# Optimization experiments

Measured on AMD Instinct MI355X. Metric: run time of the kernel, lower is better.

## Reference

```python
import jax, jax.numpy as jnp
import numpy as np

D_MODEL = 2048
HEADS = 32
HEAD_DIM = 64   # D_MODEL // HEADS
STATE = 256
KCONV = 4
CHUNK = 64
EPS = 1e-5
CONV_DIM = D_MODEL + 2 * STATE          # 2560 (n_groups=1)
PROJ = D_MODEL + CONV_DIM + HEADS       # 4640 (z | xBC | dt)
BATCH, SEQ = 2, 2048


def rmsnorm(x, w, eps=EPS):
    return x * jax.lax.rsqrt(jnp.mean(x * x, axis=-1, keepdims=True) + eps) * w


def setup_inputs() -> dict:
    key = jax.random.key(0)
    ks = jax.random.split(key, 8)
    x = jax.random.normal(ks[0], (BATCH, SEQ, D_MODEL), jnp.float32)
    norm_w = jnp.ones((D_MODEL,), jnp.float32)
    w_in = jax.random.normal(ks[1], (D_MODEL, PROJ), jnp.float32) * 0.02
    conv_w = jax.random.normal(ks[2], (CONV_DIM, KCONV), jnp.float32) * 0.2
    conv_b = jnp.zeros((CONV_DIM,), jnp.float32)
    # HF-style dt init: softplus(dt_bias) uniform-log in [1e-3, 1e-1]
    dt0 = jnp.exp(jax.random.uniform(ks[3], (HEADS,)) * (np.log(0.1) - np.log(0.001)) + np.log(0.001))
    dt_bias = dt0 + jnp.log(-jnp.expm1(-dt0))
    A_log = jnp.log(jnp.arange(1, HEADS + 1, dtype=jnp.float32))
    D_skip = jnp.ones((HEADS,), jnp.float32)
    gnorm_w = jnp.ones((D_MODEL,), jnp.float32)
    w_out = jax.random.normal(ks[4], (D_MODEL, D_MODEL), jnp.float32) * 0.02
    wo_w = jax.random.normal(ks[5], (D_MODEL, D_MODEL), jnp.float32) * 0.02
    return {"x": x, "norm_w": norm_w, "w_in": w_in, "conv_w": conv_w, "conv_b": conv_b,
            "dt_bias": dt_bias, "A_log": A_log, "D_skip": D_skip, "gnorm_w": gnorm_w,
            "w_out": w_out, "wo_w": wo_w}


def reference(x, norm_w, w_in, conv_w, conv_b, dt_bias, A_log, D_skip, gnorm_w, w_out, wo_w):
    b, L, _ = x.shape
    nc = L // CHUNK
    # pre-RMSNorm
    xn = rmsnorm(x, norm_w)
    # in_proj and split: z | xBC | dt
    proj = xn @ w_in
    z = proj[..., :D_MODEL]
    xBC = proj[..., D_MODEL:D_MODEL + CONV_DIM]
    dt = proj[..., D_MODEL + CONV_DIM:]                      # [b,L,H]
    # causal depthwise conv1d (kernel 4) + SiLU
    xp = jnp.pad(xBC, ((0, 0), (KCONV - 1, 0), (0, 0)))
    conv = conv_b + sum(xp[:, k:k + L] * conv_w[:, k] for k in range(KCONV))
    conv = jax.nn.silu(conv)
    xs = conv[..., :D_MODEL].reshape(b, L, HEADS, HEAD_DIM)  # SSM input
    Bm = conv[..., D_MODEL:D_MODEL + STATE]                  # [b,L,N] (n_groups=1)
    Cm = conv[..., D_MODEL + STATE:]                         # [b,L,N]
    dt = jax.nn.softplus(dt + dt_bias)                       # [b,L,H], >0
    A = -jnp.exp(A_log)                                      # [H]
    # ---- Mamba2 chunked selective scan (chunk_size=64) ----
    def ck(a):
        return a.reshape(b, nc, CHUNK, *a.shape[2:])
    xs_c, dt_c, B_c, C_c = ck(xs), ck(dt), ck(Bm), ck(Cm)
    Adt = dt_c * A                                           # [b,c,l,h] (<=0)
    Acs = jnp.cumsum(Adt, axis=2)
    # intra-chunk (diagonal blocks)
    seg = Acs[:, :, :, None, :] - Acs[:, :, None, :, :]      # [b,c,l,s,h]
    idx = jnp.arange(CHUNK)
    mask = (idx[:, None] >= idx[None, :])[None, None, :, :, None]
    Lmat = jnp.where(mask, jnp.exp(seg), 0.0)                # [b,c,l,s,h]
    CB = jnp.einsum('bcln,bcsn->bcls', C_c, B_c)
    xt = xs_c * dt_c[..., None]                              # [b,c,l,h,p]
    Y_diag = jnp.einsum('bclsh,bcshp->bclhp', CB[..., None] * Lmat, xt)
    # chunk-final states
    decay_states = jnp.exp(Acs[:, :, -1:, :] - Acs)          # [b,c,l,h]
    states = jnp.einsum('bcln,bclh,bclhp->bchpn', B_c, decay_states, xt)
    # inter-chunk recurrence (scan over nc chunks only)
    chunk_decay = jnp.exp(Acs[:, :, -1, :])                  # [b,c,h]
    def step(S, inp):
        dec, st = inp
        return S * dec[:, :, None, None] + st, S
    S0 = jnp.zeros((b, HEADS, HEAD_DIM, STATE), x.dtype)
    _, prev = jax.lax.scan(step, S0, (jnp.moveaxis(chunk_decay, 1, 0), jnp.moveaxis(states, 1, 0)))
    prev = jnp.moveaxis(prev, 0, 1)                          # [b,c,h,p,n] state at chunk start
    Y_off = jnp.einsum('bcln,bchpn,bclh->bclhp', C_c, prev, jnp.exp(Acs))
    y = (Y_diag + Y_off).reshape(b, L, HEADS, HEAD_DIM) + D_skip[None, None, :, None] * xs
    y = y.reshape(b, L, D_MODEL)
    # gated RMSNorm, out_proj, then wo
    y = rmsnorm(y * jax.nn.silu(z), gnorm_w)
    return (y @ w_out) @ wo_w
```

## Files before the change

kernel.cpp:

```cpp
#include <hip/hip_runtime.h>
#include <math.h>

#define D_MODEL 2048
#define HEADS 32
#define HEAD_DIM 64
#define STATE 256
#define KCONV 4
#define CHUNK 64
#define NC 32
#define SEQL 2048
#define BATCHN 2
#define CONV_DIMN 2560
#define PROJ_DIM 4640
#define PROJB_W 4608
#define EPSF 1e-5f
#define BL (BATCHN * SEQL)

typedef __attribute__((ext_vector_type(8))) short short8;
typedef __attribute__((ext_vector_type(4))) short short4v;
typedef __attribute__((ext_vector_type(4))) float f32x4;

__device__ __forceinline__ short f2bf(float f) {
  unsigned u = __builtin_bit_cast(unsigned, f);
  u = (u + 0x7fffu + ((u >> 16) & 1u)) >> 16;
  return (short)u;
}
__device__ __forceinline__ float b2f(short s) {
  unsigned u = ((unsigned)(unsigned short)s) << 16;
  return __builtin_bit_cast(float, u);
}
__device__ __forceinline__ void gld16(const void* g, void* l) {
  __builtin_amdgcn_global_load_lds((const __attribute__((address_space(1))) unsigned int*)g,
                                   (__attribute__((address_space(3))) unsigned int*)l,
                                   16, 0, 0);
}

__global__ __launch_bounds__(256) void transpose_bf16_k(const float* __restrict__ W,
                                                        short* __restrict__ WT,
                                                        int K, int ncols, int stride) {
  __shared__ float tile[32][33];
  int bn = blockIdx.x * 32, bk = blockIdx.y * 32;
  int tx = threadIdx.x & 31, ty = threadIdx.x >> 5;
  #pragma unroll
  for (int i = 0; i < 32; i += 8) {
    int k = bk + ty + i, n = bn + tx;
    tile[ty + i][tx] = (n < ncols) ? W[(size_t)k * stride + n] : 0.f;
  }
  __syncthreads();
  #pragma unroll
  for (int i = 0; i < 32; i += 8) {
    int n = bn + ty + i, k = bk + tx;
    WT[(size_t)n * K + k] = f2bf(tile[tx][ty + i]);
  }
}

__global__ __launch_bounds__(256) void dt_gemm_k(const float* __restrict__ x,
                                                 const float* __restrict__ norm_w,
                                                 const float* __restrict__ w_in,
                                                 short* __restrict__ xnb,
                                                 float* __restrict__ dtraw) {
  int row = blockIdx.x;
  int t = threadIdx.x;
  __shared__ float sx[D_MODEL];
  __shared__ float red[8][32];
  __shared__ float sred[4];
  const float4* x4 = (const float4*)(x + (size_t)row * D_MODEL);
  const float4* nw4 = (const float4*)norm_w;
  float ss = 0.f;
  for (int i = t; i < D_MODEL / 4; i += 256) {
    float4 v = x4[i];
    ss += v.x * v.x + v.y * v.y + v.z * v.z + v.w * v.w;
    float4 nw = nw4[i];
    float4 pv; pv.x = v.x * nw.x; pv.y = v.y * nw.y; pv.z = v.z * nw.z; pv.w = v.w * nw.w;
    ((float4*)sx)[i] = pv;
  }
  #pragma unroll
  for (int off = 32; off > 0; off >>= 1) ss += __shfl_down(ss, off);
  if ((t & 63) == 0) sred[t >> 6] = ss;
  __syncthreads();
  float tot = sred[0] + sred[1] + sred[2] + sred[3];
  float scale = rsqrtf(tot / (float)D_MODEL + EPSF);
  {
    float4 a = ((const float4*)sx)[2 * t], b = ((const float4*)sx)[2 * t + 1];
    short tmp[8];
    tmp[0] = f2bf(a.x * scale); tmp[1] = f2bf(a.y * scale);
    tmp[2] = f2bf(a.z * scale); tmp[3] = f2bf(a.w * scale);
    tmp[4] = f2bf(b.x * scale); tmp[5] = f2bf(b.y * scale);
    tmp[6] = f2bf(b.z * scale); tmp[7] = f2bf(b.w * scale);
    *(int4*)(xnb + (size_t)row * D_MODEL + t * 8) = *(int4*)tmp;
  }
  int h = t & 31, sl = t >> 5;
  float acc = 0.f;
  for (int k = sl * 256; k < sl * 256 + 256; k++)
    acc += sx[k] * w_in[(size_t)k * PROJ_DIM + (D_MODEL + CONV_DIMN) + h];
  red[sl][h] = acc;
  __syncthreads();
  if (t < 32) {
    float s = 0.f;
    #pragma unroll
    for (int i = 0; i < 8; i++) s += red[i][t];
    dtraw[(size_t)row * HEADS + t] = s * scale;
  }
}

template<bool BF16OUT>
__global__ __launch_bounds__(256, 2) void gemm_tw_k(const short* __restrict__ A,
                                                    const short* __restrict__ BT,
                                                    void* __restrict__ Cout,
                                                    int M, int N, int K) {
  constexpr int ABUF = 256 * 32;
  constexpr int BUFS = ABUF + 128 * 32;
  constexpr int LPT = 6;
  __shared__ short lds[3 * BUFS];

  const int t = threadIdx.x;
  const int lane = t & 63, w = t >> 6;
  const int mr = lane & 15, q = lane >> 4;
  const int cq8 = (q ^ ((mr >> 1) & 3)) * 8;
  const int stj = ((lane & 3) ^ ((lane >> 3) & 3)) * 8;
  const int str = lane >> 2;
  const int wm = w & 1, wn = w >> 1;

  const int nbx = N >> 7;
  const int nwg = nbx * (M >> 8);
  const int cpx = nwg >> 3;
  const int bid = blockIdx.x;
  const int swz = (bid & 7) * cpx + (bid >> 3);
  const int bx = swz % nbx, by = swz / nbx;
  const int m0 = by * 256, n0 = bx * 128;

  const int NT = K >> 5;
  f32x4 acc[8][4] = {};

  auto STAGE = [&](int tile, int buf) {
    short* dst = &lds[buf * BUFS];
    const int kb = tile * 32 + stj;
    #pragma unroll
    for (int cc = 0; cc < 4; cc++)
      gld16(A + (size_t)(m0 + w * 64 + cc * 16 + str) * K + kb,
            dst + (w * 64 + cc * 16) * 32);
    #pragma unroll
    for (int cc = 0; cc < 2; cc++)
      gld16(BT + (size_t)(n0 + w * 32 + cc * 16 + str) * K + kb,
            dst + ABUF + (w * 32 + cc * 16) * 32);
  };

  STAGE(0, 0); STAGE(1, 1);
  asm volatile("s_waitcnt vmcnt(%0)" :: "n"(LPT) : "memory");
  __builtin_amdgcn_s_barrier();

  int bufc = 0;
  for (int tt = 0; tt < NT; ++tt) {
    const short* sA = &lds[bufc * BUFS];
    const short* sB = sA + ABUF;
    if (tt + 2 < NT) STAGE(tt + 2, bufc >= 1 ? bufc - 1 : 2);
    short8 af[4], bfr[4];
    #pragma unroll
    for (int ni = 0; ni < 4; ni++)
      bfr[ni] = *(const short8*)&sB[(wn * 64 + ni * 16 + mr) * 32 + cq8];
    #pragma unroll
    for (int mi = 0; mi < 4; mi++)
      af[mi] = *(const short8*)&sA[(wm * 128 + mi * 16 + mr) * 32 + cq8];
    __builtin_amdgcn_s_setprio(1);
    #pragma unroll
    for (int mi = 0; mi < 4; mi++)
      #pragma unroll
      for (int ni = 0; ni < 4; ni++)
        acc[mi][ni] = __builtin_amdgcn_mfma_f32_16x16x32_bf16(af[mi], bfr[ni], acc[mi][ni], 0, 0, 0);
    __builtin_amdgcn_s_setprio(0);
    #pragma unroll
    for (int mi = 0; mi < 4; mi++)
      af[mi] = *(const short8*)&sA[(wm * 128 + 64 + mi * 16 + mr) * 32 + cq8];
    __builtin_amdgcn_s_setprio(1);
    #pragma unroll
    for (int mi = 0; mi < 4; mi++)
      #pragma unroll
      for (int ni = 0; ni < 4; ni++)
        acc[4 + mi][ni] = __builtin_amdgcn_mfma_f32_16x16x32_bf16(af[mi], bfr[ni], acc[4 + mi][ni], 0, 0, 0);
    __builtin_amdgcn_s_setprio(0);
    __builtin_amdgcn_sched_barrier(0);
    if (tt + 2 < NT) asm volatile("s_waitcnt vmcnt(%0)" :: "n"(LPT) : "memory");
    else             asm volatile("s_waitcnt vmcnt(0)" ::: "memory");
    __builtin_amdgcn_s_barrier();
    bufc = (bufc == 2) ? 0 : bufc + 1;
  }

  #pragma unroll
  for (int mi = 0; mi < 8; mi++)
    #pragma unroll
    for (int ni = 0; ni < 4; ni++) {
      const int gm = m0 + wm * 128 + ((mi & 3) + (mi >> 2) * 4) * 16 + ((mi >> 2) ? 64 - 64 : 0);
      const int gmr = m0 + wm * 128 + (mi >> 2) * 64 + (mi & 3) * 16 + q * 4;
      const int gn = n0 + wn * 64 + ni * 16 + mr;
      #pragma unroll
      for (int r = 0; r < 4; r++) {
        if (BF16OUT) ((short*)Cout)[(size_t)(gmr + r) * N + gn] = f2bf(acc[mi][ni][r]);
        else         ((float*)Cout)[(size_t)(gmr + r) * N + gn] = acc[mi][ni][r];
      }
    }
}

__global__ __launch_bounds__(256) void conv_silu_k(const short* __restrict__ projb,
                                                   const float* __restrict__ cw,
                                                   const float* __restrict__ cb,
                                                   short* __restrict__ out) {
  int idx = blockIdx.x * 256 + threadIdx.x;
  int ci = idx % (CONV_DIMN / 8);
  int bt = idx / (CONV_DIMN / 8);
  int t = bt & (SEQL - 1);
  int b = bt >> 11;
  int c = ci * 8;
  float4 w4[8];
  #pragma unroll
  for (int j = 0; j < 8; j++) w4[j] = ((const float4*)cw)[c + j];
  float acc[8];
  {
    float4 b0 = ((const float4*)(cb + c))[0], b1 = ((const float4*)(cb + c))[1];
    acc[0] = b0.x; acc[1] = b0.y; acc[2] = b0.z; acc[3] = b0.w;
    acc[4] = b1.x; acc[5] = b1.y; acc[6] = b1.z; acc[7] = b1.w;
  }
  #pragma unroll
  for (int k = 0; k < KCONV; k++) {
    int tt = t - (KCONV - 1) + k;
    if (tt < 0) continue;
    short8 v = *(const short8*)&projb[((size_t)(b * SEQL + tt)) * PROJB_W + D_MODEL + c];
    #pragma unroll
    for (int j = 0; j < 8; j++) {
      float wv = (k == 0) ? w4[j].x : (k == 1) ? w4[j].y : (k == 2) ? w4[j].z : w4[j].w;
      acc[j] += b2f(v[j]) * wv;
    }
  }
  short o[8];
  #pragma unroll
  for (int j = 0; j < 8; j++) o[j] = f2bf(acc[j] / (1.f + expf(-acc[j])));
  *(int4*)&out[(size_t)bt * CONV_DIMN + c] = *(int4*)o;
}

__global__ __launch_bounds__(256) void dt_acs_k(const float* __restrict__ dtraw,
                                                const float* __restrict__ dt_bias,
                                                const float* __restrict__ A_log,
                                                float* __restrict__ dtb, float* __restrict__ acsb) {
  int bc = blockIdx.x;
  int b = bc / NC, c = bc % NC;
  int t = threadIdx.x;
  int l = t & 63, w = t >> 6;
  size_t base = ((size_t)(b * SEQL + c * CHUNK + l)) * HEADS;
  #pragma unroll
  for (int i = 0; i < 8; i++) {
    int h = w * 8 + i;
    float raw = dtraw[base + h] + dt_bias[h];
    float dt = raw > 20.f ? raw : log1pf(expf(raw));
    float adt = -expf(A_log[h]) * dt;
    float cs = adt;
    #pragma unroll
    for (int off = 1; off < 64; off <<= 1) {
      float v = __shfl_up(cs, off);
      if (l >= off) cs += v;
    }
    dtb[base + h] = dt;
    acsb[base + h] = cs;
  }
}

__global__ __launch_bounds__(256) void cb_k(const short* __restrict__ convb,
                                            short* __restrict__ CB) {
  int bc = blockIdx.x;
  int b = bc / NC, c = bc % NC;
  __shared__ float sC[64][65];
  __shared__ float sB[64][65];
  int t = threadIdx.x;
  int s = t & 63;
  int lb = (t >> 6) * 16;
  float acc[16] = {};
  size_t rowb = ((size_t)(b * SEQL + c * CHUNK)) * CONV_DIMN;
  for (int nt = 0; nt < 4; nt++) {
    __syncthreads();
    #pragma unroll
    for (int i = 0; i < 16; i++) {
      int e = t + 256 * i;
      int r = e >> 6, col = e & 63;
      sC[r][col] = b2f(convb[rowb + (size_t)r * CONV_DIMN + (D_MODEL + STATE) + nt * 64 + col]);
      sB[r][col] = b2f(convb[rowb + (size_t)r * CONV_DIMN + D_MODEL + nt * 64 + col]);
    }
    __syncthreads();
    for (int n = 0; n < 64; n++) {
      float bv = sB[s][n];
      #pragma unroll
      for (int j = 0; j < 16; j++) acc[j] += sC[lb + j][n] * bv;
    }
  }
  size_t ob = ((size_t)bc) * 64 * 64;
  #pragma unroll
  for (int j = 0; j < 16; j++) CB[ob + (size_t)(lb + j) * 64 + s] = f2bf(acc[j]);
}

__global__ __launch_bounds__(256) void chunk_states_k(const short* __restrict__ convb,
                                                      const float* __restrict__ dtb,
                                                      const float* __restrict__ acsb,
                                                      short* __restrict__ G0,
                                                      short* __restrict__ G1) {
  int blk = blockIdx.x & 1023;
  int b = blockIdx.x >> 10;
  short* G = b ? G1 : G0;
  int h = blk & 31, c = blk >> 5;
  __shared__ __align__(16) short sXT[64][72];
  __shared__ __align__(16) short sBT[256][72];
  __shared__ float swt[64];
  int t = threadIdx.x;
  size_t rowb = ((size_t)(b * SEQL + c * CHUNK)) * CONV_DIMN;
  size_t ab = ((size_t)(b * SEQL + c * CHUNK)) * HEADS;
  if (t < 64) {
    float a = acsb[ab + (size_t)t * HEADS + h];
    float alast = acsb[ab + (size_t)63 * HEADS + h];
    swt[t] = expf(alast - a) * dtb[ab + (size_t)t * HEADS + h];
  }
  __syncthreads();
  #pragma unroll
  for (int i = 0; i < 4; i++) {
    int e = t + 256 * i;
    int l = e >> 4, p4 = (e & 15) * 4;
    short4v v = *(const short4v*)&convb[rowb + (size_t)l * CONV_DIMN + h * HEAD_DIM + p4];
    float wt = swt[l];
    short vv[4] = {v.x, v.y, v.z, v.w};
    #pragma unroll
    for (int j = 0; j < 4; j++) {
      int p = p4 + j;
      sXT[p][((((l >> 3) ^ ((p >> 2) & 7)) << 3) | (l & 7))] = f2bf(b2f(vv[j]) * wt);
    }
  }
  #pragma unroll
  for (int i = 0; i < 16; i++) {
    int e = t + 256 * i;
    int l = e >> 6, n4 = (e & 63) * 4;
    short4v v = *(const short4v*)&convb[rowb + (size_t)l * CONV_DIMN + D_MODEL + n4];
    short vv[4] = {v.x, v.y, v.z, v.w};
    #pragma unroll
    for (int j = 0; j < 4; j++) {
      int n = n4 + j;
      sBT[n][((((l >> 3) ^ ((n >> 2) & 7)) << 3) | (l & 7))] = vv[j];
    }
  }
  __syncthreads();
  int lane = t & 63, w = t >> 6;
  int mr = lane & 15, q = lane >> 4;
  f32x4 acc[4][4] = {};
  #pragma unroll
  for (int ks = 0; ks < 2; ks++) {
    short8 af[4], bfr[4];
    #pragma unroll
    for (int mi = 0; mi < 4; mi++) {
      int p = mi * 16 + mr;
      af[mi] = *(const short8*)&sXT[p][(((ks * 4 + q) ^ ((p >> 2) & 7)) << 3)];
    }
    #pragma unroll
    for (int ni = 0; ni < 4; ni++) {
      int n = w * 64 + ni * 16 + mr;
      bfr[ni] = *(const short8*)&sBT[n][(((ks * 4 + q) ^ ((n >> 2) & 7)) << 3)];
    }
    #pragma unroll
    for (int mi = 0; mi < 4; mi++)
      #pragma unroll
      for (int ni = 0; ni < 4; ni++)
        acc[mi][ni] = __builtin_amdgcn_mfma_f32_16x16x32_bf16(af[mi], bfr[ni], acc[mi][ni], 0, 0, 0);
  }
  size_t gb = (size_t)blk * (64 * 256);
  #pragma unroll
  for (int mi = 0; mi < 4; mi++)
    #pragma unroll
    for (int ni = 0; ni < 4; ni++)
      #pragma unroll
      for (int r = 0; r < 4; r++)
        G[gb + (size_t)(mi * 16 + q * 4 + r) * 256 + w * 64 + ni * 16 + mr] = f2bf(acc[mi][ni][r]);
}

__global__ __launch_bounds__(256) void scan_states_k(short* __restrict__ G0,
                                                     short* __restrict__ G1,
                                                     const float* __restrict__ acsb) {
  int gid = blockIdx.x * 256 + threadIdx.x;
  int b = gid >> 16;
  int tid = gid & 65535;
  short* G = b ? G1 : G0;
  int n8 = tid & 31, p = (tid >> 5) & 63, h = tid >> 11;
  float S[8] = {};
  for (int c = 0; c < NC; c++) {
    size_t base = (((size_t)(c * HEADS + h) * 64) + p) * 256 + n8 * 8;
    short gs[8];
    *(int4*)gs = *(const int4*)&G[base];
    short ws8[8];
    #pragma unroll
    for (int j = 0; j < 8; j++) ws8[j] = f2bf(S[j]);
    *(int4*)&G[base] = *(int4*)ws8;
    float dec = expf(acsb[((size_t)(b * SEQL + c * CHUNK + 63)) * HEADS + h]);
    #pragma unroll
    for (int j = 0; j < 8; j++) S[j] = S[j] * dec + b2f(gs[j]);
  }
}

__global__ __launch_bounds__(256) void y_fused_k(const short* __restrict__ convb,
                                                 const short* __restrict__ CBb,
                                                 const short* __restrict__ G0,
                                                 const short* __restrict__ G1,
                                                 const float* __restrict__ dtb,
                                                 const float* __restrict__ acsb,
                                                 const float* __restrict__ D_skip,
                                                 float* __restrict__ Y) {
  int blk = blockIdx.x & 1023;
  int b = blockIdx.x >> 10;
  const short* G = b ? G1 : G0;
  int h = blk & 31, c = blk >> 5;
  __shared__ __align__(16) short sM[64][72];
  __shared__ __align__(16) short sXT[64][72];
  __shared__ float sacs[64], sdt[64], sea[64];
  int t = threadIdx.x;
  int lane = t & 63, w = t >> 6;
  size_t rowb = ((size_t)(b * SEQL + c * CHUNK)) * CONV_DIMN;
  size_t ab = ((size_t)(b * SEQL + c * CHUNK)) * HEADS;
  size_t cbbase = ((size_t)(b * NC + c)) * 64 * 64;
  if (t < 64) {
    float a = acsb[ab + (size_t)t * HEADS + h];
    sacs[t] = a;
    sea[t] = expf(a);
    sdt[t] = dtb[ab + (size_t)t * HEADS + h];
  }
  __syncthreads();
  #pragma unroll
  for (int i = 0; i < 16; i++) {
    int e = t + 256 * i;
    int r = e >> 6, col = e & 63;
    float m = 0.f;
    if (col <= r)
      m = b2f(CBb[cbbase + (size_t)r * 64 + col]) * expf(sacs[r] - sacs[col]) * sdt[col];
    sM[r][col] = f2bf(m);
  }
  #pragma unroll
  for (int i = 0; i < 4; i++) {
    int e = t + 256 * i;
    int l = e >> 4, p4 = (e & 15) * 4;
    short4v v = *(const short4v*)&convb[rowb + (size_t)l * CONV_DIMN + h * HEAD_DIM + p4];
    short vv[4] = {v.x, v.y, v.z, v.w};
    #pragma unroll
    for (int j = 0; j < 4; j++) {
      int p = p4 + j;
      sXT[p][((((l >> 3) ^ ((p >> 2) & 7)) << 3) | (l & 7))] = vv[j];
    }
  }
  __syncthreads();
  int mr = lane & 15, q = lane >> 4;
  int wm = (w & 1) * 32, wn = (w >> 1) * 32;
  f32x4 acc1[2][2] = {}, acc2[2][2] = {};
  #pragma unroll
  for (int ks = 0; ks < 2; ks++) {
    short8 af[2], bfr[2];
    #pragma unroll
    for (int mi = 0; mi < 2; mi++)
      af[mi] = *(const short8*)&sM[wm + mi * 16 + mr][ks * 32 + q * 8];
    #pragma unroll
    for (int ni = 0; ni < 2; ni++) {
      int p = wn + ni * 16 + mr;
      bfr[ni] = *(const short8*)&sXT[p][(((ks * 4 + q) ^ ((p >> 2) & 7)) << 3)];
    }
    #pragma unroll
    for (int mi = 0; mi < 2; mi++)
      #pragma unroll
      for (int ni = 0; ni < 2; ni++)
        acc1[mi][ni] = __builtin_amdgcn_mfma_f32_16x16x32_bf16(af[mi], bfr[ni], acc1[mi][ni], 0, 0, 0);
  }
  const short* Crow = convb + rowb + (D_MODEL + STATE);
  size_t gbase = (size_t)blk * (64 * 256);
  #pragma unroll
  for (int st = 0; st < 8; st++) {
    short8 af[2], bfr[2];
    #pragma unroll
    for (int mi = 0; mi < 2; mi++) {
      int l = wm + mi * 16 + mr;
      af[mi] = *(const short8*)&Crow[(size_t)l * CONV_DIMN + st * 32 + q * 8];
    }
    #pragma unroll
    for (int ni = 0; ni < 2; ni++) {
      int p = wn + ni * 16 + mr;
      bfr[ni] = *(const short8*)&G[gbase + (size_t)p * 256 + st * 32 + q * 8];
    }
    #pragma unroll
    for (int mi = 0; mi < 2; mi++)
      #pragma unroll
      for (int ni = 0; ni < 2; ni++)
        acc2[mi][ni] = __builtin_amdgcn_mfma_f32_16x16x32_bf16(af[mi], bfr[ni], acc2[mi][ni], 0, 0, 0);
  }
  float dsk = D_skip[h];
  size_t ybase = ((size_t)(b * SEQL + c * CHUNK)) * D_MODEL + h * HEAD_DIM;
  #pragma unroll
  for (int mi = 0; mi < 2; mi++)
    #pragma unroll
    for (int ni = 0; ni < 2; ni++) {
      int p = wn + ni * 16 + mr;
      #pragma unroll
      for (int r = 0; r < 4; r++) {
        int l = wm + mi * 16 + q * 4 + r;
        float xsv = b2f(sXT[p][((((l >> 3) ^ ((p >> 2) & 7)) << 3) | (l & 7))]);
        Y[ybase + (size_t)l * D_MODEL + p] =
            acc1[mi][ni][r] + sea[l] * acc2[mi][ni][r] + dsk * xsv;
      }
    }
}

__global__ __launch_bounds__(256) void gated_norm_bf16_k(const float* __restrict__ Y,
                                                         const short* __restrict__ projb,
                                                         const float* __restrict__ gw,
                                                         short* __restrict__ out) {
  int row = blockIdx.x;
  int t = threadIdx.x;
  const float4* y4 = (const float4*)(Y + (size_t)row * D_MODEL);
  float4 ya = y4[2 * t], yb = y4[2 * t + 1];
  short zt[8];
  *(int4*)zt = *(const int4*)(projb + (size_t)row * PROJB_W + t * 8);
  float g[8];
  float yv[8] = {ya.x, ya.y, ya.z, ya.w, yb.x, yb.y, yb.z, yb.w};
  float ss = 0.f;
  #pragma unroll
  for (int i = 0; i < 8; i++) {
    float z = b2f(zt[i]);
    g[i] = yv[i] * (z / (1.f + expf(-z)));
    ss += g[i] * g[i];
  }
  #pragma unroll
  for (int off = 32; off > 0; off >>= 1) ss += __shfl_down(ss, off);
  __shared__ float ws_[4];
  if ((t & 63) == 0) ws_[t >> 6] = ss;
  __syncthreads();
  float tot = ws_[0] + ws_[1] + ws_[2] + ws_[3];
  float scale = rsqrtf(tot / (float)D_MODEL + EPSF);
  const float4* g4 = (const float4*)gw;
  float4 wa = g4[2 * t], wb = g4[2 * t + 1];
  float wv[8] = {wa.x, wa.y, wa.z, wa.w, wb.x, wb.y, wb.z, wb.w};
  short tmp[8];
  #pragma unroll
  for (int i = 0; i < 8; i++) tmp[i] = f2bf(g[i] * scale * wv[i]);
  *(int4*)(out + (size_t)row * D_MODEL + t * 8) = *(int4*)tmp;
}

extern "C" void kernel_launch(void* const* d_in, const int* in_sizes, int n_in,
                              void* d_out, int out_size, void* d_ws, size_t ws_size,
                              hipStream_t stream) {
  const float* x       = (const float*)d_in[0];
  const float* norm_w  = (const float*)d_in[1];
  const float* w_in    = (const float*)d_in[2];
  const float* conv_w  = (const float*)d_in[3];
  const float* conv_b  = (const float*)d_in[4];
  const float* dt_bias = (const float*)d_in[5];
  const float* A_log   = (const float*)d_in[6];
  const float* D_skip  = (const float*)d_in[7];
  const float* gnorm_w = (const float*)d_in[8];
  const float* w_out   = (const float*)d_in[9];
  const float* wo_w    = (const float*)d_in[10];
  float* out = (float*)d_out;

  float* ws    = (float*)d_ws;
  short* xnb   = (short*)ws;
  short* w_inT = (short*)(ws + 4194304);
  short* projb = (short*)(ws + 8912896);
  short* convb = (short*)(ws + 18350080);
  float* dtraw = ws + 23592960;
  float* dtb   = ws + 23724032;
  float* acsb  = ws + 23855104;
  short* CBb   = (short*)(ws + 23986176);
  float* Yb    = ws + 24117248;
  short* w_outT= (short*)(ws + 32505856);
  short* wo_wT = (short*)(ws + 34603008);
  short* G0    = (short*)ws;
  short* G1    = (short*)out;
  short* Yg    = convb;
  short* t1b   = (short*)ws;

  dt_gemm_k<<<BL, 256, 0, stream>>>(x, norm_w, w_in, xnb, dtraw);
  transpose_bf16_k<<<dim3(PROJB_W / 32, D_MODEL / 32), 256, 0, stream>>>(w_in, w_inT, D_MODEL, PROJB_W, PROJ_DIM);
  transpose_bf16_k<<<dim3(D_MODEL / 32, D_MODEL / 32), 256, 0, stream>>>(w_out, w_outT, D_MODEL, D_MODEL, D_MODEL);
  transpose_bf16_k<<<dim3(D_MODEL / 32, D_MODEL / 32), 256, 0, stream>>>(wo_w, wo_wT, D_MODEL, D_MODEL, D_MODEL);
  gemm_tw_k<true><<<(BL / 256) * (PROJB_W / 128), 256, 0, stream>>>(xnb, w_inT, projb, BL, PROJB_W, D_MODEL);
  conv_silu_k<<<(BL * (CONV_DIMN / 8)) / 256, 256, 0, stream>>>(projb, conv_w, conv_b, convb);
  dt_acs_k<<<BATCHN * NC, 256, 0, stream>>>(dtraw, dt_bias, A_log, dtb, acsb);
  cb_k<<<BATCHN * NC, 256, 0, stream>>>(convb, CBb);
  chunk_states_k<<<BATCHN * NC * HEADS, 256, 0, stream>>>(convb, dtb, acsb, G0, G1);
  scan_states_k<<<512, 256, 0, stream>>>(G0, G1, acsb);
  y_fused_k<<<BATCHN * NC * HEADS, 256, 0, stream>>>(convb, CBb, G0, G1, dtb, acsb, D_skip, Yb);
  gated_norm_bf16_k<<<BL, 256, 0, stream>>>(Yb, projb, gnorm_w, Yg);
  gemm_tw_k<true><<<(BL / 256) * (D_MODEL / 128), 256, 0, stream>>>(Yg, w_outT, t1b, BL, D_MODEL, D_MODEL);
  gemm_tw_k<false><<<(BL / 256) * (D_MODEL / 128), 256, 0, stream>>>(t1b, wo_wT, out, BL, D_MODEL, D_MODEL);
}
```

Before: 606.4 us.

## Rewrite GEMM as 8-wave 512-thread kernel with K=64 tiles and split-phase prefetch

After: 605.5 us. Within noise of the previous version (-0.2%).

```diff
diff --git a/kernel.cpp b/kernel.cpp
--- a/kernel.cpp
+++ b/kernel.cpp
@@ -104,13 +104,14 @@
 }
 
 template<bool BF16OUT>
-__global__ __launch_bounds__(256, 2) void gemm_tw_k(const short* __restrict__ A,
-                                                    const short* __restrict__ BT,
-                                                    void* __restrict__ Cout,
-                                                    int M, int N, int K) {
-  constexpr int ABUF = 256 * 32;
-  constexpr int BUFS = ABUF + 128 * 32;
-  constexpr int LPT = 6;
+__global__ __launch_bounds__(512, 1) void gemm8p_k(const short* __restrict__ A,
+                                                   const short* __restrict__ BT,
+                                                   void* __restrict__ Cout,
+                                                   int M, int N, int K) {
+  constexpr int AHALF = 8192;
+  constexpr int BHALF = 4096;
+  constexpr int ATILE = 2 * AHALF;
+  constexpr int BUFS  = ATILE + 2 * BHALF;
   __shared__ short lds[3 * BUFS];
 
   const int t = threadIdx.x;
@@ -119,7 +120,7 @@
   const int cq8 = (q ^ ((mr >> 1) & 3)) * 8;
   const int stj = ((lane & 3) ^ ((lane >> 3) & 3)) * 8;
   const int str = lane >> 2;
-  const int wm = w & 1, wn = w >> 1;
+  const int wm = w & 3, wn = w >> 2;
 
   const int nbx = N >> 7;
   const int nwg = nbx * (M >> 8);
@@ -129,73 +130,85 @@
   const int bx = swz % nbx, by = swz / nbx;
   const int m0 = by * 256, n0 = bx * 128;
 
-  const int NT = K >> 5;
-  f32x4 acc[8][4] = {};
-
-  auto STAGE = [&](int tile, int buf) {
+  const int NT = K >> 6;
+  f32x4 acc[4][4] = {};
+
+  auto STAGE_A = [&](int tile, int buf) {
     short* dst = &lds[buf * BUFS];
-    const int kb = tile * 32 + stj;
-    #pragma unroll
-    for (int cc = 0; cc < 4; cc++)
-      gld16(A + (size_t)(m0 + w * 64 + cc * 16 + str) * K + kb,
-            dst + (w * 64 + cc * 16) * 32);
-    #pragma unroll
-    for (int cc = 0; cc < 2; cc++)
-      gld16(BT + (size_t)(n0 + w * 32 + cc * 16 + str) * K + kb,
-            dst + ABUF + (w * 32 + cc * 16) * 32);
+    #pragma unroll
+    for (int s = 0; s < 2; s++) {
+      const int kb = tile * 64 + s * 32 + stj;
+      #pragma unroll
+      for (int cc = 0; cc < 2; cc++)
+        gld16(A + (size_t)(m0 + w * 32 + cc * 16 + str) * K + kb,
+              dst + s * AHALF + (w * 32 + cc * 16) * 32);
+    }
   };
-
-  STAGE(0, 0); STAGE(1, 1);
-  asm volatile("s_waitcnt vmcnt(%0)" :: "n"(LPT) : "memory");
+  auto STAGE_B = [&](int tile, int buf) {
+    short* dst = &lds[buf * BUFS + ATILE];
+    #pragma unroll
+    for (int s = 0; s < 2; s++) {
+      const int kb = tile * 64 + s * 32 + stj;
+      gld16(BT + (size_t)(n0 + w * 16 + str) * K + kb,
+            dst + s * BHALF + w * 512);
+    }
+  };
+
+  STAGE_A(0, 0); STAGE_B(0, 0);
+  STAGE_A(1, 1); STAGE_B(1, 1);
+  asm volatile("s_waitcnt vmcnt(6)" ::: "memory");
   __builtin_amdgcn_s_barrier();
 
   int bufc = 0;
   for (int tt = 0; tt < NT; ++tt) {
-    const short* sA = &lds[bufc * BUFS];
-    const short* sB = sA + ABUF;
-    if (tt + 2 < NT) STAGE(tt + 2, bufc >= 1 ? bufc - 1 : 2);
-    short8 af[4], bfr[4];
-    #pragma unroll
-    for (int ni = 0; ni < 4; ni++)
-      bfr[ni] = *(const short8*)&sB[(wn * 64 + ni * 16 + mr) * 32 + cq8];
-    #pragma unroll
-    for (int mi = 0; mi < 4; mi++)
-      af[mi] = *(const short8*)&sA[(wm * 128 + mi * 16 + mr) * 32 + cq8];
-    __builtin_amdgcn_s_setprio(1);
-    #pragma unroll
-    for (int mi = 0; mi < 4; mi++)
+    const int pb = bufc >= 1 ? bufc - 1 : 2;
+    const short* sAb = &lds[bufc * BUFS];
+    const short* sBb = sAb + ATILE;
+    const bool pf = (tt + 2 < NT);
+    #pragma unroll
+    for (int s = 0; s < 2; s++) {
+      const short* sA = sAb + s * AHALF;
+      const short* sB = sBb + s * BHALF;
+      short8 af[4], bfr[4];
+      #pragma unroll
+      for (int mi = 0; mi < 4; mi++)
+        af[mi] = *(const short8*)&sA[(wm * 64 + mi * 16 + mr) * 32 + cq8];
       #pragma unroll
       for (int ni = 0; ni < 4; ni++)
-        acc[mi][ni] = __builtin_amdgcn_mfma_f32_16x16x32_bf16(af[mi], bfr[ni], acc[mi][ni], 0, 0, 0);
-    __builtin_amdgcn_s_setprio(0);
-    #pragma unroll
-    for (int mi = 0; mi < 4; mi++)
-      af[mi] = *(const short8*)&sA[(wm * 128 + 64 + mi * 16 + mr) * 32 + cq8];
-    __builtin_amdgcn_s_setprio(1);
-    #pragma unroll
-    for (int mi = 0; mi < 4; mi++)
-      #pragma unroll
-      for (int ni = 0; ni < 4; ni++)
-        acc[4 + mi][ni] = __builtin_amdgcn_mfma_f32_16x16x32_bf16(af[mi], bfr[ni], acc[4 + mi][ni], 0, 0, 0);
-    __builtin_amdgcn_s_setprio(0);
-    __builtin_amdgcn_sched_barrier(0);
-    if (tt + 2 < NT) asm volatile("s_waitcnt vmcnt(%0)" :: "n"(LPT) : "memory");
-    else             asm volatile("s_waitcnt vmcnt(0)" ::: "memory");
-    __builtin_amdgcn_s_barrier();
+        bfr[ni] = *(const short8*)&sB[(wn * 64 + ni * 16 + mr) * 32 + cq8];
+      if (pf) { if (s == 0) STAGE_A(tt + 2, pb); else STAGE_B(tt + 2, pb); }
+      __builtin_amdgcn_s_barrier();
+      asm volatile("s_waitcnt lgkmcnt(0)" ::: "memory");
+      __builtin_amdgcn_sched_barrier(0);
+      __builtin_amdgcn_s_setprio(1);
+      #pragma unroll
+      for (int mi = 0; mi < 4; mi++)
+        #pragma unroll
+        for (int ni = 0; ni < 4; ni++)
+          acc[mi][ni] = __builtin_amdgcn_mfma_f32_16x16x32_bf16(af[mi], bfr[ni], acc[mi][ni], 0, 0, 0);
+      __builtin_amdgcn_s_setprio(0);
+      __builtin_amdgcn_sched_barrier(0);
+      if (s == 0) {
+        __builtin_amdgcn_s_barrier();
+      } else {
+        if (pf) asm volatile("s_waitcnt vmcnt(6)" ::: "memory");
+        else    asm volatile("s_waitcnt vmcnt(0)" ::: "memory");
+        __builtin_amdgcn_s_barrier();
+      }
+    }
     bufc = (bufc == 2) ? 0 : bufc + 1;
   }
 
   #pragma unroll
-  for (int mi = 0; mi < 8; mi++)
+  for (int mi = 0; mi < 4; mi++)
     #pragma unroll
     for (int ni = 0; ni < 4; ni++) {
-      const int gm = m0 + wm * 128 + ((mi & 3) + (mi >> 2) * 4) * 16 + ((mi >> 2) ? 64 - 64 : 0);
-      const int gmr = m0 + wm * 128 + (mi >> 2) * 64 + (mi & 3) * 16 + q * 4;
+      const int gm = m0 + wm * 64 + mi * 16 + q * 4;
       const int gn = n0 + wn * 64 + ni * 16 + mr;
       #pragma unroll
       for (int r = 0; r < 4; r++) {
-        if (BF16OUT) ((short*)Cout)[(size_t)(gmr + r) * N + gn] = f2bf(acc[mi][ni][r]);
-        else         ((float*)Cout)[(size_t)(gmr + r) * N + gn] = acc[mi][ni][r];
+        if (BF16OUT) ((short*)Cout)[(size_t)(gm + r) * N + gn] = f2bf(acc[mi][ni][r]);
+        else         ((float*)Cout)[(size_t)(gm + r) * N + gn] = acc[mi][ni][r];
       }
     }
 }
@@ -575,7 +588,7 @@
   transpose_bf16_k<<<dim3(PROJB_W / 32, D_MODEL / 32), 256, 0, stream>>>(w_in, w_inT, D_MODEL, PROJB_W, PROJ_DIM);
   transpose_bf16_k<<<dim3(D_MODEL / 32, D_MODEL / 32), 256, 0, stream>>>(w_out, w_outT, D_MODEL, D_MODEL, D_MODEL);
   transpose_bf16_k<<<dim3(D_MODEL / 32, D_MODEL / 32), 256, 0, stream>>>(wo_w, wo_wT, D_MODEL, D_MODEL, D_MODEL);
-  gemm_tw_k<true><<<(BL / 256) * (PROJB_W / 128), 256, 0, stream>>>(xnb, w_inT, projb, BL, PROJB_W, D_MODEL);
+  gemm8p_k<true><<<(BL / 256) * (PROJB_W / 128), 512, 0, stream>>>(xnb, w_inT, projb, BL, PROJB_W, D_MODEL);
   conv_silu_k<<<(BL * (CONV_DIMN / 8)) / 256, 256, 0, stream>>>(projb, conv_w, conv_b, convb);
   dt_acs_k<<<BATCHN * NC, 256, 0, stream>>>(dtraw, dt_bias, A_log, dtb, acsb);
   cb_k<<<BATCHN * NC, 256, 0, stream>>>(convb, CBb);
@@ -583,6 +596,6 @@
   scan_states_k<<<512, 256, 0, stream>>>(G0, G1, acsb);
   y_fused_k<<<BATCHN * NC * HEADS, 256, 0, stream>>>(convb, CBb, G0, G1, dtb, acsb, D_skip, Yb);
   gated_norm_bf16_k<<<BL, 256, 0, stream>>>(Yb, projb, gnorm_w, Yg);
-  gemm_tw_k<true><<<(BL / 256) * (D_MODEL / 128), 256, 0, stream>>>(Yg, w_outT, t1b, BL, D_MODEL, D_MODEL);
-  gemm_tw_k<false><<<(BL / 256) * (D_MODEL / 128), 256, 0, stream>>>(t1b, wo_wT, out, BL, D_MODEL, D_MODEL);
-}
+  gemm8p_k<true><<<(BL / 256) * (D_MODEL / 128), 512, 0, stream>>>(Yg, w_outT, t1b, BL, D_MODEL, D_MODEL);
+  gemm8p_k<false><<<(BL / 256) * (D_MODEL / 128), 512, 0, stream>>>(t1b, wo_wT, out, BL, D_MODEL, D_MODEL);
+}
```
